# Optimization experiments

Hardware: AMD Instinct MI355X
Metric: run time of the kernel (lower is better)

The kernel has to match this reference:

```python
import jax, jax.numpy as jnp
import numpy as np

D_IN, D, P, H, DH, DFF, L = 3072, 1024, 36, 8, 128, 2048, 6
SCALE = np.float32(1.0 / np.sqrt(DH))
# leave-one-out index matrix: row i lists all patch indices except i -> (36, 35)
LOO_IDX = jnp.asarray(np.array([[j for j in range(P) if j != i] for i in range(P)], dtype=np.int32))


def _ln(x, g, b, eps=1e-5):
    m = jnp.mean(x, axis=-1, keepdims=True)
    v = jnp.var(x, axis=-1, keepdims=True)
    return (x - m) / jnp.sqrt(v + eps) * g + b


def setup_inputs() -> dict:
    key = jax.random.key(0)
    ks = jax.random.split(key, 16)
    w = lambda k, shape: jax.random.normal(k, shape, jnp.float32) * 0.02
    return {
        "x": jax.random.normal(ks[0], (128, P, D_IN), jnp.float32),
        "ln0_g": jnp.ones((D_IN,), jnp.float32), "ln0_b": jnp.zeros((D_IN,), jnp.float32),
        "Wred": w(ks[1], (D, D_IN)), "bred": jnp.zeros((D,), jnp.float32),
        "h0_w1": w(ks[2], (64, D)), "h0_b1": jnp.zeros((64,), jnp.float32),
        "h0_w2": w(ks[3], (1, 64)), "h0_b2": jnp.zeros((1,), jnp.float32),
        "temperature": jnp.ones((1,), jnp.float32) * 0.07,
        "Wqkv": w(ks[4], (L, 3 * D, D)), "bqkv": jnp.zeros((L, 3 * D), jnp.float32),
        "Wo": w(ks[5], (L, D, D)), "bo": jnp.zeros((L, D), jnp.float32),
        "ln1_g": jnp.ones((L, D), jnp.float32), "ln1_b": jnp.zeros((L, D), jnp.float32),
        "W1": w(ks[6], (L, DFF, D)), "b1": jnp.zeros((L, DFF), jnp.float32),
        "W2": w(ks[7], (L, D, DFF)), "b2": jnp.zeros((L, D), jnp.float32),
        "ln2_g": jnp.ones((L, D), jnp.float32), "ln2_b": jnp.zeros((L, D), jnp.float32),
        "lnf_g": jnp.ones((D,), jnp.float32), "lnf_b": jnp.zeros((D,), jnp.float32),
    }


def reference(x, ln0_g, ln0_b, Wred, bred, h0_w1, h0_b1, h0_w2, h0_b2, temperature,
              Wqkv, bqkv, Wo, bo, ln1_g, ln1_b, W1, b1, W2, b2, ln2_g, ln2_b, lnf_g, lnf_b):
    B = x.shape[0]
    # dim_reduce (dropout is identity at inference)
    xr = jax.nn.gelu(_ln(x, ln0_g, ln0_b) @ Wred.T + bred, approximate=False)  # (B,P,D)

    # Leave-one-out attention maps. H0 is a pointwise (kernel_size=1) stack,
    # so each position's score is independent: compute once, then gather the
    h1 = jax.nn.gelu(jnp.einsum('bpc,oc->bpo', xr, h0_w1) + h0_b1, approximate=False)  # (B,P,64)
    full = jnp.einsum('bpo,uo->bpu', h1, h0_w2)[..., 0] + h0_b2[0]                      # (B,P)
    attention_maps = jax.nn.sigmoid(full[:, LOO_IDX] / temperature[0])                  # (B,P,P-1)

    # Pre-norm transformer encoder (PyTorch norm_first=True, relu FFN, no final encoder norm)
    y = xr
    for l in range(L):
        qkv = _ln(y, ln1_g[l], ln1_b[l]) @ Wqkv[l].T + bqkv[l]  # (B,P,3D)
        q, k, v = jnp.split(qkv, 3, axis=-1)
        q = q.reshape(B, P, H, DH).transpose(0, 2, 1, 3)
        k = k.reshape(B, P, H, DH).transpose(0, 2, 1, 3)
        v = v.reshape(B, P, H, DH).transpose(0, 2, 1, 3)
        attn = jax.nn.softmax(jnp.einsum('bhqd,bhkd->bhqk', q, k) * SCALE, axis=-1)
        o = jnp.einsum('bhqk,bhkd->bhqd', attn, v).transpose(0, 2, 1, 3).reshape(B, P, D)
        y = y + o @ Wo[l].T + bo[l]
        f = jax.nn.relu(_ln(y, ln2_g[l], ln2_b[l]) @ W1[l].T + b1[l])
        y = y + f @ W2[l].T + b2[l]

    return _ln(y, lnf_g, lnf_b), attention_maps
```

## Files before the change

### kernel.cpp

```cpp
#include <hip/hip_runtime.h>
#include <hip/hip_bf16.h>

typedef unsigned short u16;
typedef unsigned int u32;
typedef __bf16 bf16x8 __attribute__((ext_vector_type(8)));
typedef float f32x4 __attribute__((ext_vector_type(4)));

#define DEV static __device__ __forceinline__
#define GPTR(p) (const __attribute__((address_space(1))) u32*)(p)
#define LPTR(p) (__attribute__((address_space(3))) u32*)(p)

DEV float bf2f(u16 u) { return __uint_as_float((u32)u << 16); }
DEV u16 f2bf(float f) {
  u32 x = __float_as_uint(f);
  x += 0x7fffu + ((x >> 16) & 1u);
  return (u16)(x >> 16);
}
DEV float gelu_f(float x) { return 0.5f * x * (1.0f + erff(x * 0.70710678118654752440f)); }

__global__ void cvt_k(const float* __restrict__ in, u16* __restrict__ out, int n4) {
  int i = blockIdx.x * 256 + threadIdx.x;
  if (i < n4) {
    float4 v = ((const float4*)in)[i];
    ushort4 o;
    o.x = f2bf(v.x); o.y = f2bf(v.y); o.z = f2bf(v.z); o.w = f2bf(v.w);
    ((ushort4*)out)[i] = o;
  }
}

__global__ void w1t_k(const float* __restrict__ w1, float* __restrict__ w1t) {
  int i = blockIdx.x * 256 + threadIdx.x;
  if (i < 64 * 1024) {
    int o = i >> 10, c = i & 1023;
    w1t[c * 64 + o] = w1[i];
  }
}

template<int DIM, int OUTM, int INBF>
__global__ __launch_bounds__(256) void ln_k(const void* __restrict__ inp,
                                            const float* __restrict__ g,
                                            const float* __restrict__ b,
                                            void* __restrict__ outp) {
  constexpr int NV = DIM / 1024;
  const int row = blockIdx.x, tid = threadIdx.x;
  float4 v[NV];
  float s = 0.f, s2 = 0.f;
#pragma unroll
  for (int i = 0; i < NV; ++i) {
    if (INBF == 0) {
      v[i] = ((const float4*)inp)[(size_t)row * (DIM / 4) + tid + i * 256];
    } else {
      ushort4 u = ((const ushort4*)inp)[(size_t)row * (DIM / 4) + tid + i * 256];
      v[i] = make_float4(bf2f(u.x), bf2f(u.y), bf2f(u.z), bf2f(u.w));
    }
    s += v[i].x + v[i].y + v[i].z + v[i].w;
    s2 += v[i].x * v[i].x + v[i].y * v[i].y + v[i].z * v[i].z + v[i].w * v[i].w;
  }
  __shared__ float red[8];
#pragma unroll
  for (int off = 32; off; off >>= 1) { s += __shfl_down(s, off); s2 += __shfl_down(s2, off); }
  if ((tid & 63) == 0) { red[(tid >> 6) * 2] = s; red[(tid >> 6) * 2 + 1] = s2; }
  __syncthreads();
  s = red[0] + red[2] + red[4] + red[6];
  s2 = red[1] + red[3] + red[5] + red[7];
  const float mean = s / DIM;
  const float rstd = rsqrtf(s2 / DIM - mean * mean + 1e-5f);
#pragma unroll
  for (int i = 0; i < NV; ++i) {
    const int c4 = tid + i * 256;
    float4 gv = ((const float4*)g)[c4];
    float4 bv = ((const float4*)b)[c4];
    float o0 = (v[i].x - mean) * rstd * gv.x + bv.x;
    float o1 = (v[i].y - mean) * rstd * gv.y + bv.y;
    float o2 = (v[i].z - mean) * rstd * gv.z + bv.z;
    float o3 = (v[i].w - mean) * rstd * gv.w + bv.w;
    if (OUTM == 0) {
      ushort4 u4;
      u4.x = f2bf(o0); u4.y = f2bf(o1); u4.z = f2bf(o2); u4.w = f2bf(o3);
      ((ushort4*)outp)[(size_t)row * (DIM / 4) + c4] = u4;
    } else {
      ((float4*)outp)[(size_t)row * (DIM / 4) + c4] = make_float4(o0, o1, o2, o3);
    }
  }
}

template<int EPI, int BN>
__global__ __launch_bounds__(512, 4) void gemm_bt(const u16* __restrict__ A,
                                                  const u16* __restrict__ B,
                                                  const float* __restrict__ bias,
                                                  u16* __restrict__ Cb,
                                                  int N, int K, int nx) {
  constexpr int WC = BN / 32;
  constexpr int MR = (128 * WC / 8) / 16;
  __shared__ u16 As[2][128 * 64];
  __shared__ u16 Bs[2][BN * 64];
  const int tid = threadIdx.x;
  const int nwg = gridDim.x;
  const int bid = blockIdx.x;
  const int swz = (bid & 7) * (nwg >> 3) + (bid >> 3);
  const int by = swz / nx, bx = swz - by * nx;
  const int brow = by * 128, bcol = bx * BN;
  const int lane = tid & 63, w = tid >> 6;
  const int wr = (w / WC) * (MR * 16), wc = (w % WC) * 32;
  const int fr = lane & 15, fg = lane >> 4;
  const int swb = (fr & 7) << 4;
  const int ldr = lane >> 3;
  const int lc8 = lane & 7;
  const int cs8 = (lc8 ^ ldr) * 8;

  const u16* Ab = A + (size_t)(brow + ldr) * K + cs8;
  const u16* Bb = B + (size_t)(bcol + ldr) * K + cs8;

  f32x4 acc[MR][2];
  const f32x4 z = {0.f, 0.f, 0.f, 0.f};
#pragma unroll
  for (int m = 0; m < MR; ++m) { acc[m][0] = z; acc[m][1] = z; }

  auto stage = [&](int kt, int buf) {
    const int k0 = kt << 6;
#pragma unroll
    for (int i = 0; i < 2; ++i) {
      const int c = i * 8 + w;
      __builtin_amdgcn_global_load_lds(GPTR(Ab + (size_t)c * 8 * K + k0),
                                       LPTR(&As[buf][c * 512 + lane * 8]), 16, 0, 0);
    }
#pragma unroll
    for (int i = 0; i < BN / 64; ++i) {
      const int c = i * 8 + w;
      __builtin_amdgcn_global_load_lds(GPTR(Bb + (size_t)c * 8 * K + k0),
                                       LPTR(&Bs[buf][c * 512 + lane * 8]), 16, 0, 0);
    }
  };

  stage(0, 0);
  const int nkt = K >> 6;
  for (int kt = 0; kt < nkt; ++kt) {
    const int buf = kt & 1;
    asm volatile("s_waitcnt vmcnt(0)" ::: "memory");
    __builtin_amdgcn_s_barrier();
    __builtin_amdgcn_sched_barrier(0);
    if (kt + 1 < nkt) stage(kt + 1, buf ^ 1);
    const char* Asb = (const char*)&As[buf][0];
    const char* Bsb = (const char*)&Bs[buf][0];
    __builtin_amdgcn_s_setprio(1);
#pragma unroll
    for (int ks = 0; ks < 2; ++ks) {
      bf16x8 af[MR], bfr[2];
      const int cb = (ks * 64 + fg * 16) ^ swb;
#pragma unroll
      for (int m = 0; m < MR; ++m)
        af[m] = *(const bf16x8*)(Asb + (wr + m * 16 + fr) * 128 + cb);
#pragma unroll
      for (int n = 0; n < 2; ++n)
        bfr[n] = *(const bf16x8*)(Bsb + (wc + n * 16 + fr) * 128 + cb);
#pragma unroll
      for (int m = 0; m < MR; ++m)
#pragma unroll
        for (int n = 0; n < 2; ++n)
          acc[m][n] = __builtin_amdgcn_mfma_f32_16x16x32_bf16(af[m], bfr[n], acc[m][n], 0, 0, 0);
    }
    __builtin_amdgcn_s_setprio(0);
  }

#pragma unroll
  for (int n = 0; n < 2; ++n) {
    const int col = bcol + wc + n * 16 + fr;
    const float bv = bias[col];
#pragma unroll
    for (int m = 0; m < MR; ++m) {
      const int row0 = brow + wr + m * 16 + fg * 4;
#pragma unroll
      for (int j = 0; j < 4; ++j) {
        float v = acc[m][n][j] + bv;
        const size_t idx = (size_t)(row0 + j) * N + col;
        if (EPI == 0) Cb[idx] = f2bf(gelu_f(v));
        else if (EPI == 1) Cb[idx] = f2bf(v);
        else if (EPI == 2) Cb[idx] = f2bf(bf2f(Cb[idx]) + v);
        else Cb[idx] = f2bf(fmaxf(v, 0.f));
      }
    }
  }
}

__global__ __launch_bounds__(256) void attn_k(const u16* __restrict__ qkv, u16* __restrict__ o) {
  constexpr int LDQ = 136;
  __shared__ u16 Q[36 * LDQ], Kk[36 * LDQ], V[36 * LDQ];
  __shared__ float S[36][38];
  const int tid = threadIdx.x;
  const int b = blockIdx.x >> 3, h = blockIdx.x & 7;
  const size_t base = (size_t)b * 36 * 3072 + h * 128;
  for (int i = tid; i < 36 * 16; i += 256) {
    const int r = i >> 4, c = (i & 15) << 3;
    const size_t src = base + (size_t)r * 3072 + c;
    *(uint4*)&Q[r * LDQ + c] = *(const uint4*)&qkv[src];
    *(uint4*)&Kk[r * LDQ + c] = *(const uint4*)&qkv[src + 1024];
    *(uint4*)&V[r * LDQ + c] = *(const uint4*)&qkv[src + 2048];
  }
  __syncthreads();
  for (int i = tid; i < 36 * 36; i += 256) {
    const int r = i / 36, c = i - r * 36;
    float s = 0.f;
    for (int d = 0; d < 128; ++d) s += bf2f(Q[r * LDQ + d]) * bf2f(Kk[c * LDQ + d]);
    S[r][c] = s * 0.08838834764831845f;
  }
  __syncthreads();
  if (tid < 36) {
    float mx = -1e30f;
    for (int c = 0; c < 36; ++c) mx = fmaxf(mx, S[tid][c]);
    float sum = 0.f;
    for (int c = 0; c < 36; ++c) { float e = expf(S[tid][c] - mx); S[tid][c] = e; sum += e; }
    const float inv = 1.f / sum;
    for (int c = 0; c < 36; ++c) S[tid][c] *= inv;
  }
  __syncthreads();
  for (int i = tid; i < 36 * 16; i += 256) {
    const int r = i >> 4, d0 = (i & 15) << 3;
    float s[8] = {0.f, 0.f, 0.f, 0.f, 0.f, 0.f, 0.f, 0.f};
    for (int j = 0; j < 36; ++j) {
      const float p = S[r][j];
#pragma unroll
      for (int e = 0; e < 8; ++e) s[e] += p * bf2f(V[j * LDQ + d0 + e]);
    }
    uint4 pk;
    pk.x = (u32)f2bf(s[0]) | ((u32)f2bf(s[1]) << 16);
    pk.y = (u32)f2bf(s[2]) | ((u32)f2bf(s[3]) << 16);
    pk.z = (u32)f2bf(s[4]) | ((u32)f2bf(s[5]) << 16);
    pk.w = (u32)f2bf(s[6]) | ((u32)f2bf(s[7]) << 16);
    *(uint4*)&o[(size_t)(b * 36 + r) * 1024 + h * 128 + d0] = pk;
  }
}

__global__ __launch_bounds__(256) void h0_k(const u16* __restrict__ xr,
                                            const float* __restrict__ w1t,
                                            const float* __restrict__ b1,
                                            const float* __restrict__ w2,
                                            const float* __restrict__ b2v,
                                            float* __restrict__ full) {
  __shared__ float xs[1024];
  __shared__ float hp[4][64];
  const int token = blockIdx.x, tid = threadIdx.x;
  {
    ushort4 u = ((const ushort4*)(xr + (size_t)token * 1024))[tid];
    ((float4*)xs)[tid] = make_float4(bf2f(u.x), bf2f(u.y), bf2f(u.z), bf2f(u.w));
  }
  __syncthreads();
  const int w = tid >> 6, lane = tid & 63;
  float s = 0.f;
  const int c0 = w * 256;
  for (int c = c0; c < c0 + 256; ++c) s += xs[c] * w1t[c * 64 + lane];
  hp[w][lane] = s;
  __syncthreads();
  if (tid < 64) {
    float h = hp[0][tid] + hp[1][tid] + hp[2][tid] + hp[3][tid] + b1[tid];
    h = gelu_f(h);
    float v = h * w2[tid];
#pragma unroll
    for (int off = 32; off; off >>= 1) v += __shfl_down(v, off);
    if (tid == 0) full[token] = v + b2v[0];
  }
}

__global__ void am2_k(const float* __restrict__ full, const float* __restrict__ temp,
                      float* __restrict__ out) {
  const int i = blockIdx.x * 256 + threadIdx.x;
  if (i < 128 * 36 * 35) {
    const int j = i % 35;
    const int t = i / 35;
    const int p = t % 36;
    const int b = t / 36;
    const int col = j + (j >= p ? 1 : 0);
    const float v = full[b * 36 + col] / temp[0];
    out[i] = 1.f / (1.f + expf(-v));
  }
}

extern "C" void kernel_launch(void* const* d_in, const int* in_sizes, int n_in,
                              void* d_out, int out_size, void* d_ws, size_t ws_size,
                              hipStream_t stream) {
  const float* x     = (const float*)d_in[0];
  const float* ln0_g = (const float*)d_in[1];
  const float* ln0_b = (const float*)d_in[2];
  const float* Wred  = (const float*)d_in[3];
  const float* bred  = (const float*)d_in[4];
  const float* h0_w1 = (const float*)d_in[5];
  const float* h0_b1 = (const float*)d_in[6];
  const float* h0_w2 = (const float*)d_in[7];
  const float* h0_b2 = (const float*)d_in[8];
  const float* temp  = (const float*)d_in[9];
  const float* Wqkv  = (const float*)d_in[10];
  const float* bqkv  = (const float*)d_in[11];
  const float* Wo    = (const float*)d_in[12];
  const float* bo    = (const float*)d_in[13];
  const float* ln1_g = (const float*)d_in[14];
  const float* ln1_b = (const float*)d_in[15];
  const float* W1    = (const float*)d_in[16];
  const float* b1    = (const float*)d_in[17];
  const float* W2    = (const float*)d_in[18];
  const float* b2    = (const float*)d_in[19];
  const float* ln2_g = (const float*)d_in[20];
  const float* ln2_b = (const float*)d_in[21];
  const float* lnf_g = (const float*)d_in[22];
  const float* lnf_b = (const float*)d_in[23];

  char* ws = (char*)d_ws;
  size_t off = 0;
  auto alloc = [&](size_t bytes) -> void* {
    void* p = ws + off;
    off += (bytes + 255) & ~(size_t)255;
    return p;
  };
  u16* WredB  = (u16*)alloc((size_t)1024 * 3072 * 2);
  u16* WqkvB  = (u16*)alloc((size_t)6 * 3072 * 1024 * 2);
  u16* WoB    = (u16*)alloc((size_t)6 * 1024 * 1024 * 2);
  u16* W1B    = (u16*)alloc((size_t)6 * 2048 * 1024 * 2);
  u16* W2B    = (u16*)alloc((size_t)6 * 1024 * 2048 * 2);
  float* w1t  = (float*)alloc((size_t)1024 * 64 * 4);
  u16* yb     = (u16*)alloc((size_t)4608 * 1024 * 2);
  u16* big    = (u16*)alloc((size_t)4608 * 3072 * 2);
  u16* nbuf   = (u16*)alloc((size_t)4608 * 1024 * 2);
  float* fullb = (float*)alloc((size_t)4608 * 4);

  auto cvt = [&](const float* src, u16* dst, size_t n) {
    int n4 = (int)(n / 4);
    cvt_k<<<(n4 + 255) / 256, 256, 0, stream>>>(src, dst, n4);
  };
  cvt(Wred, WredB, (size_t)1024 * 3072);
  cvt(Wqkv, WqkvB, (size_t)6 * 3072 * 1024);
  cvt(Wo,   WoB,   (size_t)6 * 1024 * 1024);
  cvt(W1,   W1B,   (size_t)6 * 2048 * 1024);
  cvt(W2,   W2B,   (size_t)6 * 1024 * 2048);
  w1t_k<<<64 * 1024 / 256, 256, 0, stream>>>(h0_w1, w1t);

  ln_k<3072, 0, 0><<<4608, 256, 0, stream>>>(x, ln0_g, ln0_b, big);
  gemm_bt<0, 64><<<16 * 36, 512, 0, stream>>>(big, WredB, bred, yb, 1024, 3072, 16);
  h0_k<<<4608, 256, 0, stream>>>(yb, w1t, h0_b1, h0_w2, h0_b2, fullb);
  am2_k<<<(128 * 36 * 35 + 255) / 256, 256, 0, stream>>>(fullb, temp,
                                                         (float*)d_out + 4608 * 1024);

  for (int l = 0; l < 6; ++l) {
    ln_k<1024, 0, 1><<<4608, 256, 0, stream>>>(yb, ln1_g + l * 1024, ln1_b + l * 1024, nbuf);
    gemm_bt<1, 128><<<24 * 36, 512, 0, stream>>>(nbuf, WqkvB + (size_t)l * 3072 * 1024,
                                                 bqkv + l * 3072, big, 3072, 1024, 24);
    attn_k<<<128 * 8, 256, 0, stream>>>(big, nbuf);
    gemm_bt<2, 64><<<16 * 36, 512, 0, stream>>>(nbuf, WoB + (size_t)l * 1024 * 1024,
                                                bo + l * 1024, yb, 1024, 1024, 16);
    ln_k<1024, 0, 1><<<4608, 256, 0, stream>>>(yb, ln2_g + l * 1024, ln2_b + l * 1024, nbuf);
    gemm_bt<3, 128><<<16 * 36, 512, 0, stream>>>(nbuf, W1B + (size_t)l * 2048 * 1024,
                                                 b1 + l * 2048, big, 2048, 1024, 16);
    gemm_bt<2, 64><<<16 * 36, 512, 0, stream>>>(big, W2B + (size_t)l * 1024 * 2048,
                                                b2 + l * 1024, yb, 1024, 2048, 16);
  }
  ln_k<1024, 1, 1><<<4608, 256, 0, stream>>>(yb, lnf_g, lnf_b, d_out);
}
```

Measured before the change: 1.221 ms.

## Add 64x64-tile GEMM for N=1024 projections and batch h0 head over tokens

Measured after the change: 1.408 ms. 15.3% more time.

```diff
diff --git a/kernel.cpp b/kernel.cpp
--- a/kernel.cpp
+++ b/kernel.cpp
@@ -182,6 +182,94 @@
   }
 }
 
+template<int EPI>
+__global__ __launch_bounds__(256, 5) void gemm64(const u16* __restrict__ A,
+                                                 const u16* __restrict__ B,
+                                                 const float* __restrict__ bias,
+                                                 u16* __restrict__ Cb,
+                                                 int N, int K, int nx) {
+  __shared__ u16 As[2][64 * 64];
+  __shared__ u16 Bs[2][64 * 64];
+  const int tid = threadIdx.x;
+  const int nwg = gridDim.x, bid = blockIdx.x;
+  const int swz = (bid & 7) * (nwg >> 3) + (bid >> 3);
+  const int by = swz / nx, bx = swz - by * nx;
+  const int brow = by * 64, bcol = bx * 64;
+  const int lane = tid & 63, w = tid >> 6;
+  const int wr = (w >> 1) * 32, wc = (w & 1) * 32;
+  const int fr = lane & 15, fg = lane >> 4;
+  const int swb = (fr & 7) << 4;
+  const int srow = tid >> 3;
+  const int scol = ((tid & 7) ^ (srow & 7)) * 8;
+
+  const u16* Ab = A + (size_t)(brow + srow) * K + scol;
+  const u16* Bb = B + (size_t)(bcol + srow) * K + scol;
+
+  f32x4 acc[2][2];
+  const f32x4 z = {0.f, 0.f, 0.f, 0.f};
+  acc[0][0] = z; acc[0][1] = z; acc[1][0] = z; acc[1][1] = z;
+
+  auto stage = [&](int kt, int buf) {
+    const int k0 = kt << 6;
+#pragma unroll
+    for (int h = 0; h < 2; ++h) {
+      __builtin_amdgcn_global_load_lds(GPTR(Ab + (size_t)h * 32 * K + k0),
+                                       LPTR(&As[buf][h * 2048 + tid * 8]), 16, 0, 0);
+      __builtin_amdgcn_global_load_lds(GPTR(Bb + (size_t)h * 32 * K + k0),
+                                       LPTR(&Bs[buf][h * 2048 + tid * 8]), 16, 0, 0);
+    }
+  };
+
+  stage(0, 0);
+  const int nkt = K >> 6;
+  for (int kt = 0; kt < nkt; ++kt) {
+    const int buf = kt & 1;
+    asm volatile("s_waitcnt vmcnt(0)" ::: "memory");
+    __builtin_amdgcn_s_barrier();
+    __builtin_amdgcn_sched_barrier(0);
+    if (kt + 1 < nkt) stage(kt + 1, buf ^ 1);
+    const char* Asb = (const char*)&As[buf][0];
+    const char* Bsb = (const char*)&Bs[buf][0];
+    __builtin_amdgcn_s_setprio(1);
+#pragma unroll
+    for (int ks = 0; ks < 2; ++ks) {
+      bf16x8 af[2], bfr[2];
+      const int cb = (ks * 64 + fg * 16) ^ swb;
+#pragma unroll
+      for (int m = 0; m < 2; ++m)
+        af[m] = *(const bf16x8*)(Asb + (wr + m * 16 + fr) * 128 + cb);
+#pragma unroll
+      for (int n = 0; n < 2; ++n)
+        bfr[n] = *(const bf16x8*)(Bsb + (wc + n * 16 + fr) * 128 + cb);
+#pragma unroll
+      for (int m = 0; m < 2; ++m)
+#pragma unroll
+        for (int n = 0; n < 2; ++n)
+          acc[m][n] = __builtin_amdgcn_mfma_f32_16x16x32_bf16(af[m], bfr[n], acc[m][n], 0, 0, 0);
+    }
+    __builtin_amdgcn_s_setprio(0);
+  }
+
+#pragma unroll
+  for (int n = 0; n < 2; ++n) {
+    const int col = bcol + wc + n * 16 + fr;
+    const float bv = bias[col];
+#pragma unroll
+    for (int m = 0; m < 2; ++m) {
+      const int row0 = brow + wr + m * 16 + fg * 4;
+#pragma unroll
+      for (int j = 0; j < 4; ++j) {
+        float v = acc[m][n][j] + bv;
+        const size_t idx = (size_t)(row0 + j) * N + col;
+        if (EPI == 0) Cb[idx] = f2bf(gelu_f(v));
+        else if (EPI == 1) Cb[idx] = f2bf(v);
+        else if (EPI == 2) Cb[idx] = f2bf(bf2f(Cb[idx]) + v);
+        else Cb[idx] = f2bf(fmaxf(v, 0.f));
+      }
+    }
+  }
+}
+
 __global__ __launch_bounds__(256) void attn_k(const u16* __restrict__ qkv, u16* __restrict__ o) {
   constexpr int LDQ = 136;
   __shared__ u16 Q[36 * LDQ], Kk[36 * LDQ], V[36 * LDQ];
@@ -236,27 +324,37 @@
                                             const float* __restrict__ w2,
                                             const float* __restrict__ b2v,
                                             float* __restrict__ full) {
-  __shared__ float xs[1024];
-  __shared__ float hp[4][64];
-  const int token = blockIdx.x, tid = threadIdx.x;
-  {
-    ushort4 u = ((const ushort4*)(xr + (size_t)token * 1024))[tid];
-    ((float4*)xs)[tid] = make_float4(bf2f(u.x), bf2f(u.y), bf2f(u.z), bf2f(u.w));
+  __shared__ float xs[8][1024];
+  const int t0 = blockIdx.x * 8, tid = threadIdx.x;
+#pragma unroll
+  for (int i = 0; i < 8; ++i) {
+    const int idx = tid + i * 256;
+    const int t = idx >> 8, c4 = idx & 255;
+    ushort4 u = ((const ushort4*)(xr + (size_t)(t0 + t) * 1024))[c4];
+    xs[t][c4 * 4 + 0] = bf2f(u.x);
+    xs[t][c4 * 4 + 1] = bf2f(u.y);
+    xs[t][c4 * 4 + 2] = bf2f(u.z);
+    xs[t][c4 * 4 + 3] = bf2f(u.w);
   }
   __syncthreads();
   const int w = tid >> 6, lane = tid & 63;
-  float s = 0.f;
-  const int c0 = w * 256;
-  for (int c = c0; c < c0 + 256; ++c) s += xs[c] * w1t[c * 64 + lane];
-  hp[w][lane] = s;
-  __syncthreads();
-  if (tid < 64) {
-    float h = hp[0][tid] + hp[1][tid] + hp[2][tid] + hp[3][tid] + b1[tid];
-    h = gelu_f(h);
-    float v = h * w2[tid];
-#pragma unroll
-    for (int off = 32; off; off >>= 1) v += __shfl_down(v, off);
-    if (tid == 0) full[token] = v + b2v[0];
+  float s0 = 0.f, s1 = 0.f;
+  for (int c = 0; c < 1024; ++c) {
+    const float wv = w1t[c * 64 + lane];
+    s0 = fmaf(xs[w * 2 + 0][c], wv, s0);
+    s1 = fmaf(xs[w * 2 + 1][c], wv, s1);
+  }
+  const float bb = b1[lane], wo = w2[lane];
+  float v0 = gelu_f(s0 + bb) * wo;
+  float v1 = gelu_f(s1 + bb) * wo;
+#pragma unroll
+  for (int off = 32; off; off >>= 1) {
+    v0 += __shfl_down(v0, off);
+    v1 += __shfl_down(v1, off);
+  }
+  if (lane == 0) {
+    full[t0 + w * 2 + 0] = v0 + b2v[0];
+    full[t0 + w * 2 + 1] = v1 + b2v[0];
   }
 }
 
@@ -332,8 +430,8 @@
   w1t_k<<<64 * 1024 / 256, 256, 0, stream>>>(h0_w1, w1t);
 
   ln_k<3072, 0, 0><<<4608, 256, 0, stream>>>(x, ln0_g, ln0_b, big);
-  gemm_bt<0, 64><<<16 * 36, 512, 0, stream>>>(big, WredB, bred, yb, 1024, 3072, 16);
-  h0_k<<<4608, 256, 0, stream>>>(yb, w1t, h0_b1, h0_w2, h0_b2, fullb);
+  gemm64<0><<<72 * 16, 256, 0, stream>>>(big, WredB, bred, yb, 1024, 3072, 16);
+  h0_k<<<576, 256, 0, stream>>>(yb, w1t, h0_b1, h0_w2, h0_b2, fullb);
   am2_k<<<(128 * 36 * 35 + 255) / 256, 256, 0, stream>>>(fullb, temp,
                                                          (float*)d_out + 4608 * 1024);
 
@@ -342,13 +440,13 @@
     gemm_bt<1, 128><<<24 * 36, 512, 0, stream>>>(nbuf, WqkvB + (size_t)l * 3072 * 1024,
                                                  bqkv + l * 3072, big, 3072, 1024, 24);
     attn_k<<<128 * 8, 256, 0, stream>>>(big, nbuf);
-    gemm_bt<2, 64><<<16 * 36, 512, 0, stream>>>(nbuf, WoB + (size_t)l * 1024 * 1024,
-                                                bo + l * 1024, yb, 1024, 1024, 16);
+    gemm64<2><<<72 * 16, 256, 0, stream>>>(nbuf, WoB + (size_t)l * 1024 * 1024,
+                                           bo + l * 1024, yb, 1024, 1024, 16);
     ln_k<1024, 0, 1><<<4608, 256, 0, stream>>>(yb, ln2_g + l * 1024, ln2_b + l * 1024, nbuf);
     gemm_bt<3, 128><<<16 * 36, 512, 0, stream>>>(nbuf, W1B + (size_t)l * 2048 * 1024,
                                                  b1 + l * 2048, big, 2048, 1024, 16);
-    gemm_bt<2, 64><<<16 * 36, 512, 0, stream>>>(big, W2B + (size_t)l * 1024 * 2048,
-                                                b2 + l * 1024, yb, 1024, 2048, 16);
+    gemm64<2><<<72 * 16, 256, 0, stream>>>(big, W2B + (size_t)l * 1024 * 2048,
+                                           b2 + l * 1024, yb, 1024, 2048, 16);
   }
   ln_k<1024, 1, 1><<<4608, 256, 0, stream>>>(yb, lnf_g, lnf_b, d_out);
 }
```
